# Kernel tuning notes

Hardware: AMD Instinct MI355X
Metric: run time of the kernel (lower is better)

The kernel has to match this reference:

```python
import jax, jax.numpy as jnp
import numpy as np

D_MODEL = 512
D_HEAD = 64
N_HEADS = D_MODEL // D_HEAD  # 8
KSIZE = 7


def setup_inputs() -> dict:
    key = jax.random.key(0)
    k1, k2, k3 = jax.random.split(key, 3)
    x = jax.random.normal(k1, (2, 48, 48, D_MODEL), dtype=jnp.float32)
    # torch Linear(d, 3d, bias=False): y = x @ W.T ; store transposed weight directly
    w_qkv = jax.random.normal(k2, (D_MODEL, 3 * D_MODEL), dtype=jnp.float32) * 0.02
    w_out = jax.random.normal(k3, (D_MODEL, D_MODEL), dtype=jnp.float32) * 0.02
    return {"x": x, "w_qkv": w_qkv, "w_out": w_out}


def _nbhd_idx(L, k):
    # NATTEN semantics: window centered at each pixel, shifted (clamped) to stay
    # fully inside the image near borders. Returns [L, k] absolute indices.
    start = jnp.clip(jnp.arange(L) - k // 2, 0, L - k)
    return start[:, None] + jnp.arange(k)[None, :]


def reference(x, w_qkv, w_out):
    n, h, w, _ = x.shape
    qkv = (x @ w_qkv).reshape(n, h, w, 3, N_HEADS, D_HEAD)
    qkv = jnp.transpose(qkv, (3, 0, 4, 1, 2, 5))  # [3, n, nh, h, w, e]
    q, k, v = qkv[0], qkv[1], qkv[2]
    q = q / jnp.asarray(D_HEAD, q.dtype) ** 0.5

    ih = _nbhd_idx(h, KSIZE)  # [h, k]
    iw = _nbhd_idx(w, KSIZE)  # [w, k]
    IH = ih[:, None, :, None]  # [h,1,k,1]
    IW = iw[None, :, None, :]  # [1,w,1,k]

    # gather per-pixel 2D neighborhoods: [n, nh, h, w, ka, kb, e]
    k_nb = k[:, :, IH, IW, :]
    logits = jnp.einsum('nghwe,nghwabe->nghwab', q, k_nb)
    logits = logits.reshape(n, N_HEADS, h, w, KSIZE * KSIZE)
    attn = jax.nn.softmax(logits, axis=-1).reshape(n, N_HEADS, h, w, KSIZE, KSIZE)

    v_nb = v[:, :, IH, IW, :]
    o = jnp.einsum('nghwab,nghwabe->nghwe', attn, v_nb)  # [n, nh, h, w, e]
    o = jnp.transpose(o, (0, 2, 3, 1, 4)).reshape(n, h, w, N_HEADS * D_HEAD)
    return o @ w_out
```

## Files before the change

### kernel.cpp

```cpp
#include <hip/hip_runtime.h>
#include <hip/hip_bf16.h>

typedef __bf16 bf16x8 __attribute__((ext_vector_type(8)));
typedef float f32x4 __attribute__((ext_vector_type(4)));

#define N_PIX 4608
#define D_MODEL 512
#define QKV_N 1536

__device__ __forceinline__ void gload_lds16(const void* g, void* l) {
  __builtin_amdgcn_global_load_lds(
      (const __attribute__((address_space(1))) unsigned int*)g,
      (__attribute__((address_space(3))) unsigned int*)l, 16, 0, 0);
}


__global__ __launch_bounds__(256) void f32_to_bf16_kernel(
    const float* __restrict__ src, __bf16* __restrict__ dst, int n) {
  int i = (blockIdx.x * 256 + threadIdx.x) * 4;
  if (i + 3 < n) {
    float4 v = *(const float4*)&src[i];
    dst[i + 0] = (__bf16)v.x;
    dst[i + 1] = (__bf16)v.y;
    dst[i + 2] = (__bf16)v.z;
    dst[i + 3] = (__bf16)v.w;
  }
}

__global__ __launch_bounds__(256) void transpose_to_bf16_kernel(
    const float* __restrict__ src, __bf16* __restrict__ dst, int R, int C) {
  __shared__ float tile[32][33];
  int bx = blockIdx.x * 32;
  int by = blockIdx.y * 32;
  int tx = threadIdx.x;
  int ty = threadIdx.y;
#pragma unroll
  for (int i = 0; i < 32; i += 8)
    tile[ty + i][tx] = src[(by + ty + i) * C + bx + tx];
  __syncthreads();
#pragma unroll
  for (int i = 0; i < 32; i += 8)
    dst[(bx + ty + i) * R + by + tx] = (__bf16)tile[tx][ty + i];
}

__global__ __launch_bounds__(256) void gemm128_kernel(
    const __bf16* __restrict__ A, const __bf16* __restrict__ Bt,
    void* __restrict__ C, int M, int N, int K, int c_is_f32) {
  __shared__ __bf16 sA[128 * 32];
  __shared__ __bf16 sB[128 * 32];
  int tid = threadIdx.x;
  int wv = tid >> 6, lane = tid & 63;
  int quad = lane >> 4, r16 = lane & 15;
  int m0 = blockIdx.y * 128, n0 = blockIdx.x * 128;

  int rA = lane >> 2;
  int kc = (lane & 3) * 8;
  const __bf16* Ag0 = A + (long)(m0 + wv * 32 + rA) * K + kc;
  const __bf16* Ag1 = Ag0 + (long)16 * K;
  const __bf16* Bg0 = Bt + (long)(n0 + wv * 32 + rA) * K + kc;
  const __bf16* Bg1 = Bg0 + (long)16 * K;
  __bf16* sA0 = &sA[(wv * 32) * 32];
  __bf16* sA1 = &sA[(wv * 32 + 16) * 32];
  __bf16* sB0 = &sB[(wv * 32) * 32];
  __bf16* sB1 = &sB[(wv * 32 + 16) * 32];

  int mw = (wv & 1) * 64, nw = (wv >> 1) * 64;

  f32x4 acc[4][4];
#pragma unroll
  for (int mt = 0; mt < 4; ++mt)
#pragma unroll
    for (int nt = 0; nt < 4; ++nt) acc[mt][nt] = f32x4{0.f, 0.f, 0.f, 0.f};

  for (int k0 = 0; k0 < K; k0 += 32) {
    __syncthreads();
    gload_lds16(Ag0 + k0, sA0);
    gload_lds16(Ag1 + k0, sA1);
    gload_lds16(Bg0 + k0, sB0);
    gload_lds16(Bg1 + k0, sB1);
    __syncthreads();
    bf16x8 af[4], bfr[4];
#pragma unroll
    for (int mt = 0; mt < 4; ++mt)
      af[mt] = *(const bf16x8*)&sA[(mw + mt * 16 + r16) * 32 + quad * 8];
#pragma unroll
    for (int nt = 0; nt < 4; ++nt)
      bfr[nt] = *(const bf16x8*)&sB[(nw + nt * 16 + r16) * 32 + quad * 8];
#pragma unroll
    for (int mt = 0; mt < 4; ++mt)
#pragma unroll
      for (int nt = 0; nt < 4; ++nt)
        acc[mt][nt] = __builtin_amdgcn_mfma_f32_16x16x32_bf16(af[mt], bfr[nt], acc[mt][nt], 0, 0, 0);
  }

  __bf16* Cb = (__bf16*)C;
  float* Cf = (float*)C;
#pragma unroll
  for (int mt = 0; mt < 4; ++mt)
#pragma unroll
    for (int r = 0; r < 4; ++r) {
      int row = m0 + mw + mt * 16 + quad * 4 + r;
#pragma unroll
      for (int nt = 0; nt < 4; ++nt) {
        int col = n0 + nw + nt * 16 + r16;
        float v = acc[mt][nt][r];
        if (c_is_f32) Cf[(long)row * N + col] = v;
        else          Cb[(long)row * N + col] = (__bf16)v;
      }
    }
}

#define KSTR 72
__global__ __launch_bounds__(256) void natten_attn_kernel(
    const __bf16* __restrict__ qkv, __bf16* __restrict__ o) {
  __shared__ __bf16 sK[196 * KSTR];
  __shared__ __bf16 sV[196 * KSTR];
  int tid = threadIdx.x;
  int bid = blockIdx.x;
  int nB = bid / 288;
  int rem = bid - nB * 288;
  int head = rem / 36;
  int tile = rem - head * 36;
  int tr = tile / 6, tc = tile - tr * 6;
  int r0 = tr * 8, c0 = tc * 8;
  int loH = r0 - 3; loH = loH < 0 ? 0 : (loH > 41 ? 41 : loH);
  int loW = c0 - 3; loW = loW < 0 ? 0 : (loW > 41 ? 41 : loW);

  for (int j = tid; j < 196 * 8; j += 256) {
    int rowi = j >> 3, ch = j & 7;
    int rr = rowi / 14, cc = rowi - rr * 14;
    int hh = loH + rr; hh = hh > 47 ? 47 : hh;
    int wp = loW + cc; wp = wp > 47 ? 47 : wp;
    long base = (long)(nB * 2304 + hh * 48 + wp) * QKV_N + head * 64 + ch * 8;
    *(uint4*)&sK[rowi * KSTR + ch * 8] = *(const uint4*)&qkv[base + 512];
    *(uint4*)&sV[rowi * KSTR + ch * 8] = *(const uint4*)&qkv[base + 1024];
  }
  __syncthreads();

  int q = tid >> 2, s = tid & 3;
  int qr = q >> 3, qc = q & 7;
  int h = r0 + qr, w = c0 + qc;
  int pix = nB * 2304 + h * 48 + w;
  int hs = h - 3; hs = hs < 0 ? 0 : (hs > 41 ? 41 : hs); hs -= loH;
  int ws = w - 3; ws = ws < 0 ? 0 : (ws > 41 ? 41 : ws); ws -= loW;
  int base = (hs * 14 + ws) * KSTR + s * 16;

  const bf16x8* qp = (const bf16x8*)&qkv[(long)pix * QKV_N + head * 64 + s * 16];
  bf16x8 q0 = qp[0], q1 = qp[1];
  float qf[16];
#pragma unroll
  for (int t = 0; t < 8; ++t) {
    qf[t] = (float)q0[t] * 0.125f;
    qf[8 + t] = (float)q1[t] * 0.125f;
  }

  float lg[49];
#pragma unroll
  for (int j = 0; j < 49; ++j) {
    int a = j / 7, b = j % 7;
    const bf16x8* kp = (const bf16x8*)&sK[base + (a * 14 + b) * KSTR];
    bf16x8 k0 = kp[0], k1 = kp[1];
    float acc = 0.f;
#pragma unroll
    for (int t = 0; t < 8; ++t) {
      acc = fmaf(qf[t], (float)k0[t], acc);
      acc = fmaf(qf[8 + t], (float)k1[t], acc);
    }
    acc += __shfl_xor(acc, 1);
    acc += __shfl_xor(acc, 2);
    lg[j] = acc;
  }

  float mx = lg[0];
#pragma unroll
  for (int j = 1; j < 49; ++j) mx = fmaxf(mx, lg[j]);
  float sm = 0.f;
#pragma unroll
  for (int j = 0; j < 49; ++j) { lg[j] = __expf(lg[j] - mx); sm += lg[j]; }
  float inv = 1.f / sm;

  float ov[16];
#pragma unroll
  for (int t = 0; t < 16; ++t) ov[t] = 0.f;
#pragma unroll
  for (int j = 0; j < 49; ++j) {
    int a = j / 7, b = j % 7;
    float pj = lg[j] * inv;
    const bf16x8* vp = (const bf16x8*)&sV[base + (a * 14 + b) * KSTR];
    bf16x8 v0 = vp[0], v1 = vp[1];
#pragma unroll
    for (int t = 0; t < 8; ++t) {
      ov[t] = fmaf(pj, (float)v0[t], ov[t]);
      ov[8 + t] = fmaf(pj, (float)v1[t], ov[8 + t]);
    }
  }

  bf16x8 o0, o1;
#pragma unroll
  for (int t = 0; t < 8; ++t) {
    o0[t] = (__bf16)ov[t];
    o1[t] = (__bf16)ov[8 + t];
  }
  bf16x8* op = (bf16x8*)&o[(long)pix * D_MODEL + head * 64 + s * 16];
  op[0] = o0;
  op[1] = o1;
}


extern "C" void kernel_launch(void* const* d_in, const int* in_sizes, int n_in,
                              void* d_out, int out_size, void* d_ws, size_t ws_size,
                              hipStream_t stream) {
  const float* x = (const float*)d_in[0];
  const float* w_qkv = (const float*)d_in[1];
  const float* w_out = (const float*)d_in[2];
  float* out = (float*)d_out;

  __bf16* ws = (__bf16*)d_ws;
  __bf16* xbf   = ws;
  __bf16* wqkvT = xbf + N_PIX * D_MODEL;
  __bf16* woutT = wqkvT + QKV_N * D_MODEL;
  __bf16* qkvb  = woutT + D_MODEL * D_MODEL;
  __bf16* obf   = qkvb + N_PIX * QKV_N;

  f32_to_bf16_kernel<<<N_PIX * D_MODEL / 1024, 256, 0, stream>>>(x, xbf, N_PIX * D_MODEL);
  transpose_to_bf16_kernel<<<dim3(QKV_N / 32, D_MODEL / 32), dim3(32, 8), 0, stream>>>(
      w_qkv, wqkvT, D_MODEL, QKV_N);
  transpose_to_bf16_kernel<<<dim3(D_MODEL / 32, D_MODEL / 32), dim3(32, 8), 0, stream>>>(
      w_out, woutT, D_MODEL, D_MODEL);
  gemm128_kernel<<<dim3(QKV_N / 128, N_PIX / 128), 256, 0, stream>>>(
      xbf, wqkvT, qkvb, N_PIX, QKV_N, D_MODEL, 0);
  natten_attn_kernel<<<576, 256, 0, stream>>>(qkvb, obf);
  gemm128_kernel<<<dim3(D_MODEL / 128, N_PIX / 128), 256, 0, stream>>>(
      obf, woutT, out, N_PIX, D_MODEL, D_MODEL, 1);
}
```

Measured before the change: 131.1 us.

## Double-buffer GEMM LDS, narrow output GEMM tile, fuse prep kernels

The GEMM now double-buffers its LDS tiles, so the next K-slice is loaded while the current one feeds the MFMAs, and one barrier per iteration is removed. The GEMM is templated on tile width, and the output projection uses 64-wide tiles so the grid has twice as many blocks to fill the GPU. The three conversion and transpose kernels are merged into a single launch with vectorised bf16 stores. LDS use per block doubles, and the single barrier relies on it waiting for the async LDS loads to finish.

```diff
diff --git a/kernel.cpp b/kernel.cpp
--- a/kernel.cpp
+++ b/kernel.cpp
@@ -1,6 +1,7 @@
 #include <hip/hip_runtime.h>
 #include <hip/hip_bf16.h>
 
+typedef __bf16 bf16x4 __attribute__((ext_vector_type(4)));
 typedef __bf16 bf16x8 __attribute__((ext_vector_type(8)));
 typedef float f32x4 __attribute__((ext_vector_type(4)));
 
@@ -14,26 +15,28 @@
       (__attribute__((address_space(3))) unsigned int*)l, 16, 0, 0);
 }
 
-
-__global__ __launch_bounds__(256) void f32_to_bf16_kernel(
-    const float* __restrict__ src, __bf16* __restrict__ dst, int n) {
-  int i = (blockIdx.x * 256 + threadIdx.x) * 4;
-  if (i + 3 < n) {
-    float4 v = *(const float4*)&src[i];
-    dst[i + 0] = (__bf16)v.x;
-    dst[i + 1] = (__bf16)v.y;
-    dst[i + 2] = (__bf16)v.z;
-    dst[i + 3] = (__bf16)v.w;
-  }
-}
-
-__global__ __launch_bounds__(256) void transpose_to_bf16_kernel(
-    const float* __restrict__ src, __bf16* __restrict__ dst, int R, int C) {
+__global__ __launch_bounds__(256) void prep_kernel(
+    const float* __restrict__ x, const float* __restrict__ wq,
+    const float* __restrict__ wo, __bf16* __restrict__ xbf,
+    __bf16* __restrict__ wqT, __bf16* __restrict__ woT) {
+  int b = blockIdx.x, tid = threadIdx.x;
+  if (b < 2304) {
+    int i = b * 1024 + tid * 4;
+    float4 v = *(const float4*)&x[i];
+    bf16x4 o = {(__bf16)v.x, (__bf16)v.y, (__bf16)v.z, (__bf16)v.w};
+    *(bf16x4*)&xbf[i] = o;
+    return;
+  }
   __shared__ float tile[32][33];
-  int bx = blockIdx.x * 32;
-  int by = blockIdx.y * 32;
-  int tx = threadIdx.x;
-  int ty = threadIdx.y;
+  const float* src; __bf16* dst; int R, C, bx, by;
+  if (b < 3072) {
+    int t = b - 2304; src = wq; dst = wqT; R = 512; C = 1536;
+    bx = (t % 48) * 32; by = (t / 48) * 32;
+  } else {
+    int t = b - 3072; src = wo; dst = woT; R = 512; C = 512;
+    bx = (t & 15) * 32; by = (t >> 4) * 32;
+  }
+  int tx = tid & 31, ty = tid >> 5;
 #pragma unroll
   for (int i = 0; i < 32; i += 8)
     tile[ty + i][tx] = src[(by + ty + i) * C + bx + tx];
@@ -43,54 +46,59 @@
     dst[(bx + ty + i) * R + by + tx] = (__bf16)tile[tx][ty + i];
 }
 
+template <int BN>
 __global__ __launch_bounds__(256) void gemm128_kernel(
     const __bf16* __restrict__ A, const __bf16* __restrict__ Bt,
     void* __restrict__ C, int M, int N, int K, int c_is_f32) {
-  __shared__ __bf16 sA[128 * 32];
-  __shared__ __bf16 sB[128 * 32];
+  constexpr int NT = BN / 32;
+  constexpr int BROWS = BN / 4;
+  __shared__ __bf16 sA[2][128 * 32];
+  __shared__ __bf16 sB[2][BN * 32];
   int tid = threadIdx.x;
   int wv = tid >> 6, lane = tid & 63;
   int quad = lane >> 4, r16 = lane & 15;
-  int m0 = blockIdx.y * 128, n0 = blockIdx.x * 128;
+  int m0 = blockIdx.y * 128, n0 = blockIdx.x * BN;
 
   int rA = lane >> 2;
   int kc = (lane & 3) * 8;
   const __bf16* Ag0 = A + (long)(m0 + wv * 32 + rA) * K + kc;
   const __bf16* Ag1 = Ag0 + (long)16 * K;
-  const __bf16* Bg0 = Bt + (long)(n0 + wv * 32 + rA) * K + kc;
-  const __bf16* Bg1 = Bg0 + (long)16 * K;
-  __bf16* sA0 = &sA[(wv * 32) * 32];
-  __bf16* sA1 = &sA[(wv * 32 + 16) * 32];
-  __bf16* sB0 = &sB[(wv * 32) * 32];
-  __bf16* sB1 = &sB[(wv * 32 + 16) * 32];
-
-  int mw = (wv & 1) * 64, nw = (wv >> 1) * 64;
-
-  f32x4 acc[4][4];
+  const __bf16* Bg0 = Bt + (long)(n0 + wv * BROWS + rA) * K + kc;
+
+  int mw = (wv & 1) * 64, nw = (wv >> 1) * (BN / 2);
+
+  f32x4 acc[4][NT];
 #pragma unroll
   for (int mt = 0; mt < 4; ++mt)
 #pragma unroll
-    for (int nt = 0; nt < 4; ++nt) acc[mt][nt] = f32x4{0.f, 0.f, 0.f, 0.f};
-
+    for (int nt = 0; nt < NT; ++nt) acc[mt][nt] = f32x4{0.f, 0.f, 0.f, 0.f};
+
+  auto stage = [&](int buf, int k0) {
+    gload_lds16(Ag0 + k0, &sA[buf][(wv * 32) * 32]);
+    gload_lds16(Ag1 + k0, &sA[buf][(wv * 32 + 16) * 32]);
+    gload_lds16(Bg0 + k0, &sB[buf][(wv * BROWS) * 32]);
+    if (BROWS == 32)
+      gload_lds16(Bg0 + (long)16 * K + k0, &sB[buf][(wv * BROWS + 16) * 32]);
+  };
+
+  stage(0, 0);
+  int cur = 0;
   for (int k0 = 0; k0 < K; k0 += 32) {
     __syncthreads();
-    gload_lds16(Ag0 + k0, sA0);
-    gload_lds16(Ag1 + k0, sA1);
-    gload_lds16(Bg0 + k0, sB0);
-    gload_lds16(Bg1 + k0, sB1);
-    __syncthreads();
-    bf16x8 af[4], bfr[4];
+    if (k0 + 32 < K) stage(cur ^ 1, k0 + 32);
+    bf16x8 af[4], bfr[NT];
 #pragma unroll
     for (int mt = 0; mt < 4; ++mt)
-      af[mt] = *(const bf16x8*)&sA[(mw + mt * 16 + r16) * 32 + quad * 8];
-#pragma unroll
-    for (int nt = 0; nt < 4; ++nt)
-      bfr[nt] = *(const bf16x8*)&sB[(nw + nt * 16 + r16) * 32 + quad * 8];
+      af[mt] = *(const bf16x8*)&sA[cur][(mw + mt * 16 + r16) * 32 + quad * 8];
+#pragma unroll
+    for (int nt = 0; nt < NT; ++nt)
+      bfr[nt] = *(const bf16x8*)&sB[cur][(nw + nt * 16 + r16) * 32 + quad * 8];
 #pragma unroll
     for (int mt = 0; mt < 4; ++mt)
 #pragma unroll
-      for (int nt = 0; nt < 4; ++nt)
+      for (int nt = 0; nt < NT; ++nt)
         acc[mt][nt] = __builtin_amdgcn_mfma_f32_16x16x32_bf16(af[mt], bfr[nt], acc[mt][nt], 0, 0, 0);
+    cur ^= 1;
   }
 
   __bf16* Cb = (__bf16*)C;
@@ -101,7 +109,7 @@
     for (int r = 0; r < 4; ++r) {
       int row = m0 + mw + mt * 16 + quad * 4 + r;
 #pragma unroll
-      for (int nt = 0; nt < 4; ++nt) {
+      for (int nt = 0; nt < NT; ++nt) {
         int col = n0 + nw + nt * 16 + r16;
         float v = acc[mt][nt][r];
         if (c_is_f32) Cf[(long)row * N + col] = v;
@@ -222,14 +230,10 @@
   __bf16* qkvb  = woutT + D_MODEL * D_MODEL;
   __bf16* obf   = qkvb + N_PIX * QKV_N;
 
-  f32_to_bf16_kernel<<<N_PIX * D_MODEL / 1024, 256, 0, stream>>>(x, xbf, N_PIX * D_MODEL);
-  transpose_to_bf16_kernel<<<dim3(QKV_N / 32, D_MODEL / 32), dim3(32, 8), 0, stream>>>(
-      w_qkv, wqkvT, D_MODEL, QKV_N);
-  transpose_to_bf16_kernel<<<dim3(D_MODEL / 32, D_MODEL / 32), dim3(32, 8), 0, stream>>>(
-      w_out, woutT, D_MODEL, D_MODEL);
-  gemm128_kernel<<<dim3(QKV_N / 128, N_PIX / 128), 256, 0, stream>>>(
+  prep_kernel<<<3328, 256, 0, stream>>>(x, w_qkv, w_out, xbf, wqkvT, woutT);
+  gemm128_kernel<128><<<dim3(QKV_N / 128, N_PIX / 128), 256, 0, stream>>>(
       xbf, wqkvT, qkvb, N_PIX, QKV_N, D_MODEL, 0);
   natten_attn_kernel<<<576, 256, 0, stream>>>(qkvb, obf);
-  gemm128_kernel<<<dim3(D_MODEL / 128, N_PIX / 128), 256, 0, stream>>>(
+  gemm128_kernel<64><<<dim3(D_MODEL / 64, N_PIX / 128), 256, 0, stream>>>(
       obf, woutT, out, N_PIX, D_MODEL, D_MODEL, 1);
 }
```

New measurement: 124.3 us. 1.05x faster.
